# Kernel optimization log

Hardware: AMD Instinct MI355X
Metric: run time of the kernel (lower is better)

The kernel has to match this reference:

```python
import jax, jax.numpy as jnp
import numpy as np
import math

N_EMBD = 1024
N_HEAD = 16
N_CTX = 2048
SCALE = True
NEG = 1e10


def setup_inputs() -> dict:
    key = jax.random.key(0)
    ks = jax.random.split(key, 4)
    B, S = 2, 2048
    x = jax.random.normal(ks[0], (B, S, N_EMBD), dtype=jnp.float32)
    c_attn_w = jax.random.normal(ks[1], (N_EMBD, 3 * N_EMBD), dtype=jnp.float32) * 0.02
    c_attn_b = jnp.zeros((3 * N_EMBD,), dtype=jnp.float32)
    c_proj_w = jax.random.normal(ks[2], (N_EMBD, N_EMBD), dtype=jnp.float32) * 0.02
    c_proj_b = jnp.zeros((N_EMBD,), dtype=jnp.float32)
    return {"x": x, "c_attn_w": c_attn_w, "c_attn_b": c_attn_b,
            "c_proj_w": c_proj_w, "c_proj_b": c_proj_b}


def reference(x, c_attn_w, c_attn_b, c_proj_w, c_proj_b):
    B, S, D = x.shape
    H = N_HEAD
    hd = D // H
    qkv = x @ c_attn_w + c_attn_b                      # [B,S,3D]
    q, k, v = jnp.split(qkv, 3, axis=-1)
    # split heads -> [B,H,S,hd]
    q = q.reshape(B, S, H, hd).transpose(0, 2, 1, 3)
    k = k.reshape(B, S, H, hd).transpose(0, 2, 1, 3)
    v = v.reshape(B, S, H, hd).transpose(0, 2, 1, 3)
    w = jnp.einsum('bhqd,bhkd->bhqk', q, k)           # [B,H,S,S]
    if SCALE:
        w = w / math.sqrt(hd)
    # multiplicative causal mask trick: w*b - 1e10*(1-b)
    b = jnp.tril(jnp.ones((S, S), dtype=w.dtype))[None, None]
    w = w * b - NEG * (1.0 - b)
    w = jax.nn.softmax(w, axis=-1)
    a = jnp.einsum('bhqk,bhkd->bhqd', w, v)           # [B,H,S,hd]
    a = a.transpose(0, 2, 1, 3).reshape(B, S, D)      # merge heads
    a = a @ c_proj_w + c_proj_b
    present = jnp.stack((k, v))                       # [2,B,H,S,hd]
    return a, present
```

## Files before the change

### kernel.cpp

```cpp
#include <hip/hip_runtime.h>
#include <hip/hip_bf16.h>
#include <cstdint>
#include <cstddef>

#define SEQ 2048
#define DMODEL 1024
#define NHEAD 16
#define HDIM 64
#define MTOT 4096
#define NQKV 3072
#define KDIM 1024

#define OUT_K_BASE  4194304u
#define OUT_V_BASE  8388608u

#define QSCALE 0.18033688011112043f

typedef __attribute__((ext_vector_type(4))) float f32x4;
typedef __attribute__((ext_vector_type(8))) __bf16 bf16x8;
typedef __attribute__((ext_vector_type(8))) short s16x8;
typedef __attribute__((ext_vector_type(4))) short s16x4;
typedef __attribute__((ext_vector_type(2))) int i32x2;

static __device__ __forceinline__ unsigned short f2bf(float f) {
  unsigned int u = __builtin_bit_cast(unsigned int, f);
  u += 0x7FFFu + ((u >> 16) & 1u);
  return (unsigned short)(u >> 16);
}

static __device__ __forceinline__ s16x4 pack4(float4 v) {
  s16x4 r;
  r[0] = (short)f2bf(v.x);
  r[1] = (short)f2bf(v.y);
  r[2] = (short)f2bf(v.z);
  r[3] = (short)f2bf(v.w);
  return r;
}

static __device__ __forceinline__ int cvtpk(float lo, float hi) {
  int r;
  asm("v_cvt_pk_bf16_f32 %0, %1, %2" : "=v"(r) : "v"(lo), "v"(hi));
  return r;
}

static __device__ __forceinline__ f32x4 mfma16(s16x8 a, s16x8 b, f32x4 c) {
  return __builtin_amdgcn_mfma_f32_16x16x32_bf16(
      __builtin_bit_cast(bf16x8, a), __builtin_bit_cast(bf16x8, b), c, 0, 0, 0);
}

static __device__ __forceinline__ void gload16(const void* g, void* l) {
  __builtin_amdgcn_global_load_lds(
      (const __attribute__((address_space(1))) unsigned int*)(uintptr_t)g,
      (__attribute__((address_space(3))) unsigned int*)(uintptr_t)l,
      16, 0, 0);
}

#define WAITVM(n) asm volatile("s_waitcnt vmcnt(" #n ")" ::: "memory")

__global__ __launch_bounds__(256) void convert_x(
    const float* __restrict__ X, unsigned short* __restrict__ Xbf)
{
  int i = blockIdx.x * 256 + threadIdx.x;
  float4 v = reinterpret_cast<const float4*>(X)[i];
  reinterpret_cast<s16x4*>(Xbf)[i] = pack4(v);
}

__global__ __launch_bounds__(256) void convert_wt(
    const float* __restrict__ W, unsigned short* __restrict__ Wt, int N)
{
  __shared__ unsigned short t[64][72];
  const int n0 = blockIdx.x * 64, k0 = blockIdx.y * 64;
  const int tid = threadIdx.x;
#pragma unroll
  for (int i = 0; i < 4; ++i) {
    int f = tid + (i << 8);
    int r = f >> 4, c4 = (f & 15) << 2;
    float4 v = *reinterpret_cast<const float4*>(&W[(size_t)(k0 + r) * N + n0 + c4]);
    *reinterpret_cast<s16x4*>(&t[r][c4]) = pack4(v);
  }
  __syncthreads();
#pragma unroll
  for (int i = 0; i < 2; ++i) {
    int g = tid + (i << 8);
    int n = g >> 3, k8 = (g & 7) << 3;
    s16x8 o;
#pragma unroll
    for (int jj = 0; jj < 8; ++jj) o[jj] = (short)t[k8 + jj][n];
    *reinterpret_cast<s16x8*>(&Wt[(size_t)(n0 + n) * KDIM + k0 + k8]) = o;
  }
}

__global__ __launch_bounds__(512, 2) void qkv_gemm(
    const unsigned short* __restrict__ Xbf,
    const unsigned short* __restrict__ Wt,
    const float* __restrict__ Bias,
    float* out,
    unsigned short* __restrict__ Qbf)
{
  __shared__ __align__(16) unsigned short lds_a[2][256][32];
  __shared__ __align__(16) unsigned short lds_b[2][256][32];

  unsigned short* Kbf = (unsigned short*)out;
  unsigned short* Vt  = Kbf + 4194304;

  const int tid = threadIdx.x;
  const int lane = tid & 63;
  const int wv = tid >> 6;
  const int wr = wv >> 2;
  const int wc = wv & 3;
  const int m0 = blockIdx.x * 256;
  const int n0 = blockIdx.y * 256;
  const int lr = lane & 15;
  const int gq = lane >> 4;

  const f32x4 fzero = {0.f, 0.f, 0.f, 0.f};
  f32x4 acc[8][4];
#pragma unroll
  for (int i = 0; i < 8; ++i)
#pragma unroll
    for (int j = 0; j < 4; ++j) acc[i][j] = fzero;

  {
    const int r0 = tid >> 2;
    const int r1 = r0 + 128;
    const int c0 = tid & 3;
    const int sc0 = ((c0 ^ ((r0 >> 1) & 3)) << 3);
    const int sc1 = ((c0 ^ ((r1 >> 1) & 3)) << 3);
    const int ub0 = (wv << 6) << 3;
    const int ub1 = ((1 << 9) + (wv << 6)) << 3;
    auto stage = [&](int nb, int kk) {
      gload16(&Xbf[(size_t)(m0 + r0) * KDIM + kk + sc0], &lds_a[nb][0][0] + ub0);
      gload16(&Xbf[(size_t)(m0 + r1) * KDIM + kk + sc1], &lds_a[nb][0][0] + ub1);
      gload16(&Wt[(size_t)(n0 + r0) * KDIM + kk + sc0], &lds_b[nb][0][0] + ub0);
      gload16(&Wt[(size_t)(n0 + r1) * KDIM + kk + sc1], &lds_b[nb][0][0] + ub1);
    };
    stage(0, 0);
    stage(1, 32);
    for (int t = 0; t < 32; ++t) {
      if (t < 31) { WAITVM(4); } else { WAITVM(0); }
      __builtin_amdgcn_s_barrier();
      const int bufg = t & 1;
      s16x8 bfv[4];
#pragma unroll
      for (int ni = 0; ni < 4; ++ni) {
        int row = wc * 64 + ni * 16 + lr;
        bfv[ni] = *reinterpret_cast<const s16x8*>(
            &lds_b[bufg][row][(gq ^ ((row >> 1) & 3)) << 3]);
      }
      __builtin_amdgcn_s_setprio(1);
#pragma unroll
      for (int mi = 0; mi < 8; ++mi) {
        int row = wr * 128 + mi * 16 + lr;
        s16x8 af = *reinterpret_cast<const s16x8*>(
            &lds_a[bufg][row][(gq ^ ((row >> 1) & 3)) << 3]);
#pragma unroll
        for (int ni = 0; ni < 4; ++ni)
          acc[mi][ni] = mfma16(af, bfv[ni], acc[mi][ni]);
      }
      __builtin_amdgcn_s_setprio(0);
      __builtin_amdgcn_s_barrier();
      if (t < 30) stage(bufg, (t + 2) << 5);
    }
  }

  const int seg = n0 >> 10;

  if (seg == 0) {
#pragma unroll
    for (int ni = 0; ni < 4; ++ni) {
      int c = n0 + wc * 64 + ni * 16 + lr;
      float bias = Bias[c];
      int h = (c & 1023) >> 6, d = c & 63;
#pragma unroll
      for (int mi = 0; mi < 8; ++mi)
#pragma unroll
        for (int j = 0; j < 4; ++j) {
          int m = m0 + wr * 128 + mi * 16 + gq * 4 + j;
          int b = m >> 11, s = m & 2047;
          Qbf[(size_t)((b * NHEAD + h) * SEQ + s) * HDIM + d] =
              f2bf((acc[mi][ni][j] + bias) * QSCALE);
        }
    }
  } else if (seg == 1) {
#pragma unroll
    for (int ni = 0; ni < 4; ++ni) {
      int c = n0 + wc * 64 + ni * 16 + lr;
      float bias = Bias[c];
      int h = (c & 1023) >> 6, d = c & 63;
#pragma unroll
      for (int mi = 0; mi < 8; ++mi)
#pragma unroll
        for (int j = 0; j < 4; ++j) {
          int m = m0 + wr * 128 + mi * 16 + gq * 4 + j;
          int b = m >> 11, s = m & 2047;
          float val = acc[mi][ni][j] + bias;
          size_t idx = (size_t)((b * NHEAD + h) * SEQ + s) * HDIM + d;
          out[OUT_K_BASE + idx] = val;
          Kbf[idx] = f2bf(val);
        }
    }
  } else {
    __syncthreads();
    unsigned short* T = (wv < 4) ? (&lds_a[0][0][0] + (wv << 12))
                                 : (&lds_b[0][0][0] + ((wv - 4) << 12));
    const int b = m0 >> 11;
    const int s0 = (m0 & 2047) + wr * 128;
    const int h = (n0 >> 6) - 32 + wc;
#pragma unroll
    for (int h2 = 0; h2 < 2; ++h2) {
#pragma unroll
      for (int ni = 0; ni < 4; ++ni) {
        int c = n0 + wc * 64 + ni * 16 + lr;
        float bias = Bias[c];
        int d_loc = ni * 16 + lr;
        int dsw = d_loc & 7;
#pragma unroll
        for (int mh = 0; mh < 4; ++mh) {
          int mi = h2 * 4 + mh;
#pragma unroll
          for (int j = 0; j < 4; ++j) {
            int s_loc = mi * 16 + gq * 4 + j;
            int ss = s_loc - (h2 << 6);
            float val = acc[mi][ni][j] + bias;
            out[OUT_V_BASE +
                (size_t)((b * NHEAD + h) * SEQ + s0 + s_loc) * HDIM + d_loc] = val;
            T[d_loc * 64 + (((ss >> 3) ^ dsw) << 3) + (ss & 7)] = f2bf(val);
          }
        }
      }
#pragma unroll
      for (int it = 0; it < 8; ++it) {
        int dl = (lane >> 3) + (it << 3);
        int cl = lane & 7;
        s16x8 vv = *reinterpret_cast<const s16x8*>(
            &T[dl * 64 + ((cl ^ (dl & 7)) << 3)]);
        size_t vi = (((size_t)(b * NHEAD + h) * HDIM + dl) << 11) +
                    s0 + (h2 << 6) + (cl << 3);
        *reinterpret_cast<s16x8*>(&Vt[vi]) = vv;
      }
    }
  }
}

__global__ __launch_bounds__(256) void proj_gemm(
    const unsigned short* __restrict__ Abf,
    const unsigned short* __restrict__ Wpt,
    const float* __restrict__ Bias,
    float* __restrict__ out)
{
  __shared__ __align__(16) unsigned short lds_a[2][128][64];
  __shared__ __align__(16) unsigned short lds_b[2][128][64];

  const int tid = threadIdx.x;
  const int lane = tid & 63;
  const int wv = tid >> 6;
  const int wr = wv >> 1, wc = wv & 1;
  const int m0 = blockIdx.x * 128;
  const int n0 = blockIdx.y * 128;
  const int lr = lane & 15;
  const int gq = lane >> 4;

  const f32x4 fzero = {0.f, 0.f, 0.f, 0.f};
  f32x4 acc[4][4];
#pragma unroll
  for (int i = 0; i < 4; ++i)
#pragma unroll
    for (int j = 0; j < 4; ++j) acc[i][j] = fzero;

  {
    const int r0 = tid >> 3;
    const int c0 = tid & 7;
    auto stage = [&](int nb, int kk) {
#pragma unroll
      for (int i = 0; i < 4; ++i) {
        int r = r0 + (i << 5);
        int sc = ((c0 ^ (r & 7)) << 3);
        int ub = (((i << 8) + (wv << 6)) << 3);
        gload16(&Abf[(size_t)(m0 + r) * KDIM + kk + sc], &lds_a[nb][0][0] + ub);
        gload16(&Wpt[(size_t)(n0 + r) * KDIM + kk + sc], &lds_b[nb][0][0] + ub);
      }
    };
    stage(0, 0);
    stage(1, 64);
    for (int t = 0; t < 16; ++t) {
      if (t < 15) { WAITVM(8); } else { WAITVM(0); }
      __builtin_amdgcn_s_barrier();
      const int bufg = t & 1;
      __builtin_amdgcn_s_setprio(1);
#pragma unroll
      for (int kf = 0; kf < 2; ++kf) {
        s16x8 bfv[4];
#pragma unroll
        for (int ni = 0; ni < 4; ++ni) {
          int row = wc * 64 + ni * 16 + lr;
          bfv[ni] = *reinterpret_cast<const s16x8*>(
              &lds_b[bufg][row][((kf * 4 + gq) ^ (row & 7)) << 3]);
        }
#pragma unroll
        for (int mi = 0; mi < 4; ++mi) {
          int row = wr * 64 + mi * 16 + lr;
          s16x8 af = *reinterpret_cast<const s16x8*>(
              &lds_a[bufg][row][((kf * 4 + gq) ^ (row & 7)) << 3]);
#pragma unroll
          for (int ni = 0; ni < 4; ++ni)
            acc[mi][ni] = mfma16(af, bfv[ni], acc[mi][ni]);
        }
      }
      __builtin_amdgcn_s_setprio(0);
      __builtin_amdgcn_s_barrier();
      if (t < 14) stage(bufg, (t + 2) << 6);
    }
  }

#pragma unroll
  for (int ni = 0; ni < 4; ++ni) {
    int c = n0 + wc * 64 + ni * 16 + lr;
    float bias = Bias[c];
#pragma unroll
    for (int mi = 0; mi < 4; ++mi) {
#pragma unroll
      for (int j = 0; j < 4; ++j) {
        int m = m0 + wr * 64 + mi * 16 + gq * 4 + j;
        out[(size_t)m * DMODEL + c] = acc[mi][ni][j] + bias;
      }
    }
  }
}

__global__ __launch_bounds__(256, 4) void attn_fwd(
    const unsigned short* __restrict__ Qbf,
    const unsigned short* __restrict__ Kbf,
    const unsigned short* __restrict__ Vtg,
    unsigned short* __restrict__ Abf)
{
  __shared__ __align__(16) unsigned short K_lds[2][64][64];
  __shared__ __align__(16) unsigned short V_lds[2][64][64];
  __shared__ __align__(16) unsigned short P_lds[4][16][64];

  const int tid = threadIdx.x;
  const int lane = tid & 63;
  const int wv = tid >> 6;
  const int bid = blockIdx.x;
  const int qt = 31 - (bid >> 5);
  const int bh = bid & 31;

  const int lr = lane & 15;
  const int gq = lane >> 4;

  const unsigned short* Kg = Kbf + (size_t)bh * (SEQ * HDIM);
  const unsigned short* Vg = Vtg + (size_t)bh * (SEQ * HDIM);
  const unsigned short* Qg = Qbf + (size_t)bh * (SEQ * HDIM)
                                 + (size_t)(qt * 64 + wv * 16) * HDIM;

  s16x8 qf0 = *reinterpret_cast<const s16x8*>(&Qg[lr * 64 + (gq << 3)]);
  s16x8 qf1 = *reinterpret_cast<const s16x8*>(&Qg[lr * 64 + 32 + (gq << 3)]);

  const f32x4 fzero = {0.f, 0.f, 0.f, 0.f};
  f32x4 O[4];
  float mrow = -1e30f, lrow = 0.f;
#pragma unroll
  for (int no = 0; no < 4; ++no) O[no] = fzero;

#define STAGE(kv0, nb)                                                        \
  {                                                                           \
    _Pragma("unroll")                                                         \
    for (int i = 0; i < 2; ++i) {                                             \
      int L = tid + (i << 8);                                                 \
      int r = L >> 3, c = L & 7;                                              \
      int cc = (c ^ (r & 7)) << 3;                                            \
      int ubase = ((i << 8) + (wv << 6)) << 3;                                \
      gload16(&Kg[(((kv0) + r) << 6) + cc], &K_lds[nb][0][0] + ubase);        \
      gload16(&Vg[((size_t)r << 11) + (kv0) + cc], &V_lds[nb][0][0] + ubase); \
    }                                                                         \
  }

  STAGE(0, 0);

  for (int t = 0; t <= qt; ++t) {
    __syncthreads();
    if (t < qt) STAGE((t + 1) * 64, (t + 1) & 1);
    const int buf = t & 1;

    f32x4 sc[4];
#pragma unroll
    for (int ni = 0; ni < 4; ++ni) {
      int kr = ni * 16 + lr;
      int sw = kr & 7;
      s16x8 kb0 = *reinterpret_cast<const s16x8*>(&K_lds[buf][kr][(gq ^ sw) << 3]);
      s16x8 kb1 = *reinterpret_cast<const s16x8*>(&K_lds[buf][kr][((gq + 4) ^ sw) << 3]);
      f32x4 tacc = mfma16(kb0, qf0, fzero);
      sc[ni] = mfma16(kb1, qf1, tacc);
    }

    if (t == qt) {
      int qloc = wv * 16 + lr;
#pragma unroll
      for (int ni = 0; ni < 4; ++ni)
#pragma unroll
        for (int r = 0; r < 4; ++r)
          if (ni * 16 + gq * 4 + r > qloc) sc[ni][r] = -1e30f;
    }

    float tmax = fmaxf(fmaxf(fmaxf(sc[0][0], sc[0][1]), fmaxf(sc[0][2], sc[0][3])),
                       fmaxf(fmaxf(sc[1][0], sc[1][1]), fmaxf(sc[1][2], sc[1][3])));
    tmax = fmaxf(tmax,
                 fmaxf(fmaxf(fmaxf(sc[2][0], sc[2][1]), fmaxf(sc[2][2], sc[2][3])),
                       fmaxf(fmaxf(sc[3][0], sc[3][1]), fmaxf(sc[3][2], sc[3][3]))));
    tmax = fmaxf(tmax, __shfl_xor(tmax, 16));
    tmax = fmaxf(tmax, __shfl_xor(tmax, 32));
    float newm = fmaxf(mrow, tmax);
    float fs = __builtin_amdgcn_exp2f(mrow - newm);
    mrow = newm;
    float rs = 0.f;
#pragma unroll
    for (int ni = 0; ni < 4; ++ni) {
#pragma unroll
      for (int r = 0; r < 4; ++r) {
        float p = __builtin_amdgcn_exp2f(sc[ni][r] - newm);
        sc[ni][r] = p;
        rs += p;
      }
    }
    rs += __shfl_xor(rs, 16);
    rs += __shfl_xor(rs, 32);
    lrow = lrow * fs + rs;
#pragma unroll
    for (int no = 0; no < 4; ++no) O[no] *= fs;

    {
      unsigned short* Prow = &P_lds[wv][lr][0];
      const int swl = lr & 7;
#pragma unroll
      for (int ni = 0; ni < 4; ++ni) {
        i32x2 d2;
        d2[0] = cvtpk(sc[ni][0], sc[ni][1]);
        d2[1] = cvtpk(sc[ni][2], sc[ni][3]);
        int off = ((((2 * ni) + (gq >> 1)) ^ swl) << 3) + ((gq & 1) << 2);
        *reinterpret_cast<i32x2*>(&Prow[off]) = d2;
      }
      s16x8 pB0 = *reinterpret_cast<const s16x8*>(&Prow[(gq ^ swl) << 3]);
      s16x8 pB1 = *reinterpret_cast<const s16x8*>(&Prow[((gq + 4) ^ swl) << 3]);

#pragma unroll
      for (int no = 0; no < 4; ++no) {
        int dr = no * 16 + lr;
        int sw = dr & 7;
        s16x8 vb0 = *reinterpret_cast<const s16x8*>(&V_lds[buf][dr][(gq ^ sw) << 3]);
        s16x8 vb1 = *reinterpret_cast<const s16x8*>(&V_lds[buf][dr][((gq + 4) ^ sw) << 3]);
        O[no] = mfma16(vb0, pB0, O[no]);
        O[no] = mfma16(vb1, pB1, O[no]);
      }
    }
  }

  const int b = bh >> 4, h = bh & 15;
  float inv = 1.0f / lrow;
  int srow = qt * 64 + wv * 16 + lr;
  size_t base = (size_t)(b * SEQ + srow) * DMODEL + h * 64 + (gq << 2);
#pragma unroll
  for (int no = 0; no < 4; ++no) {
    s16x4 ov;
#pragma unroll
    for (int r = 0; r < 4; ++r) ov[r] = (short)f2bf(O[no][r] * inv);
    *reinterpret_cast<s16x4*>(&Abf[base + no * 16]) = ov;
  }
#undef STAGE
}

extern "C" void kernel_launch(void* const* d_in, const int* in_sizes, int n_in,
                              void* d_out, int out_size, void* d_ws, size_t ws_size,
                              hipStream_t stream) {
  const float* x        = (const float*)d_in[0];
  const float* c_attn_w = (const float*)d_in[1];
  const float* c_attn_b = (const float*)d_in[2];
  const float* c_proj_w = (const float*)d_in[3];
  const float* c_proj_b = (const float*)d_in[4];
  float* out = (float*)d_out;

  unsigned short* Qbf = (unsigned short*)d_ws;
  unsigned short* Xbf = Qbf + 4194304;
  unsigned short* Abf = Xbf;
  unsigned short* Wt  = Qbf + 8388608;
  unsigned short* Wpt = Wt;
  unsigned short* Kbf = (unsigned short*)out;
  unsigned short* Vt  = Kbf + 4194304;

  convert_x<<<dim3(4096), 256, 0, stream>>>(x, Xbf);
  convert_wt<<<dim3(48, 16), 256, 0, stream>>>(c_attn_w, Wt, NQKV);
  qkv_gemm<<<dim3(16, 12), 512, 0, stream>>>(Xbf, Wt, c_attn_b, out, Qbf);
  convert_wt<<<dim3(16, 16), 256, 0, stream>>>(c_proj_w, Wpt, DMODEL);
  attn_fwd<<<dim3(1024), 256, 0, stream>>>(Qbf, Kbf, Vt, Abf);
  proj_gemm<<<dim3(32, 8), 256, 0, stream>>>(Abf, Wpt, c_proj_b, out);
}
```

Before: 113.4 us.

## Triple-buffer QKV GEMM LDS and interleave staged loads with MFMA phases

Moves the QKV GEMM main loop from double to triple buffering in LDS. Each k-step is split into two half-phases that read LDS fragments, issue part of the next-next tile's global-to-LDS loads, and then run the MFMAs between barriers. The aim is to hide global load latency and spread load issue across compute. In exchange, LDS use rises from 64KB to 96KB per block, which may block two blocks per CU, and each k-step now carries more barriers. The epilogue's LDS transpose scratch pointers are remapped to the new array sizes.

```diff
diff --git a/kernel.cpp b/kernel.cpp
--- a/kernel.cpp
+++ b/kernel.cpp
@@ -56,6 +56,7 @@
 }
 
 #define WAITVM(n) asm volatile("s_waitcnt vmcnt(" #n ")" ::: "memory")
+#define SBAR() asm volatile("s_barrier" ::: "memory")
 
 __global__ __launch_bounds__(256) void convert_x(
     const float* __restrict__ X, unsigned short* __restrict__ Xbf)
@@ -97,8 +98,8 @@
     float* out,
     unsigned short* __restrict__ Qbf)
 {
-  __shared__ __align__(16) unsigned short lds_a[2][256][32];
-  __shared__ __align__(16) unsigned short lds_b[2][256][32];
+  __shared__ __align__(16) unsigned short lds_a[3][256][32];
+  __shared__ __align__(16) unsigned short lds_b[3][256][32];
 
   unsigned short* Kbf = (unsigned short*)out;
   unsigned short* Vt  = Kbf + 4194304;
@@ -121,45 +122,68 @@
     for (int j = 0; j < 4; ++j) acc[i][j] = fzero;
 
   {
-    const int r0 = tid >> 2;
-    const int r1 = r0 + 128;
-    const int c0 = tid & 3;
-    const int sc0 = ((c0 ^ ((r0 >> 1) & 3)) << 3);
-    const int sc1 = ((c0 ^ ((r1 >> 1) & 3)) << 3);
-    const int ub0 = (wv << 6) << 3;
-    const int ub1 = ((1 << 9) + (wv << 6)) << 3;
-    auto stage = [&](int nb, int kk) {
-      gload16(&Xbf[(size_t)(m0 + r0) * KDIM + kk + sc0], &lds_a[nb][0][0] + ub0);
-      gload16(&Xbf[(size_t)(m0 + r1) * KDIM + kk + sc1], &lds_a[nb][0][0] + ub1);
-      gload16(&Wt[(size_t)(n0 + r0) * KDIM + kk + sc0], &lds_b[nb][0][0] + ub0);
-      gload16(&Wt[(size_t)(n0 + r1) * KDIM + kk + sc1], &lds_b[nb][0][0] + ub1);
+    const int sr  = tid >> 2;
+    const int ssc = ((tid & 3) ^ ((sr >> 1) & 3)) << 3;
+    const int ub  = (wv << 6) << 3;
+
+    auto stageA = [&](int nb, int kt) {
+      int kk = kt << 5;
+      gload16(&Xbf[(size_t)(m0 + sr) * KDIM + kk + ssc],
+              &lds_a[nb][0][0] + ub);
+      gload16(&Xbf[(size_t)(m0 + 128 + sr) * KDIM + kk + ssc],
+              &lds_a[nb][128][0] + ub);
     };
-    stage(0, 0);
-    stage(1, 32);
-    for (int t = 0; t < 32; ++t) {
-      if (t < 31) { WAITVM(4); } else { WAITVM(0); }
-      __builtin_amdgcn_s_barrier();
-      const int bufg = t & 1;
-      s16x8 bfv[4];
-#pragma unroll
-      for (int ni = 0; ni < 4; ++ni) {
-        int row = wc * 64 + ni * 16 + lr;
-        bfv[ni] = *reinterpret_cast<const s16x8*>(
-            &lds_b[bufg][row][(gq ^ ((row >> 1) & 3)) << 3]);
-      }
-      __builtin_amdgcn_s_setprio(1);
-#pragma unroll
-      for (int mi = 0; mi < 8; ++mi) {
-        int row = wr * 128 + mi * 16 + lr;
-        s16x8 af = *reinterpret_cast<const s16x8*>(
-            &lds_a[bufg][row][(gq ^ ((row >> 1) & 3)) << 3]);
-#pragma unroll
-        for (int ni = 0; ni < 4; ++ni)
-          acc[mi][ni] = mfma16(af, bfv[ni], acc[mi][ni]);
-      }
-      __builtin_amdgcn_s_setprio(0);
-      __builtin_amdgcn_s_barrier();
-      if (t < 30) stage(bufg, (t + 2) << 5);
+    auto stageB = [&](int nb, int kt) {
+      int kk = kt << 5;
+      gload16(&Wt[(size_t)(n0 + sr) * KDIM + kk + ssc],
+              &lds_b[nb][0][0] + ub);
+      gload16(&Wt[(size_t)(n0 + 128 + sr) * KDIM + kk + ssc],
+              &lds_b[nb][128][0] + ub);
+    };
+
+    stageA(0, 0); stageB(0, 0);
+    stageA(1, 1); stageB(1, 1);
+    WAITVM(4);
+    SBAR();
+
+    int buf = 0;
+    int sbuf = 2;
+    for (int kt = 0; kt < 32; ++kt) {
+#pragma unroll
+      for (int q = 0; q < 2; ++q) {
+        s16x8 af[4], bfv[4];
+#pragma unroll
+        for (int ml = 0; ml < 4; ++ml) {
+          int row = wr * 128 + (q * 4 + ml) * 16 + lr;
+          af[ml] = *reinterpret_cast<const s16x8*>(
+              &lds_a[buf][row][(gq ^ ((row >> 1) & 3)) << 3]);
+        }
+#pragma unroll
+        for (int ni = 0; ni < 4; ++ni) {
+          int row = wc * 64 + ni * 16 + lr;
+          bfv[ni] = *reinterpret_cast<const s16x8*>(
+              &lds_b[buf][row][(gq ^ ((row >> 1) & 3)) << 3]);
+        }
+        if (kt < 30) {
+          if (q == 0) stageA(sbuf, kt + 2);
+          else        stageB(sbuf, kt + 2);
+        }
+        if (q == 1) {
+          if (kt < 30)       { WAITVM(4); }
+          else if (kt == 30) { WAITVM(0); }
+        }
+        SBAR();
+        __builtin_amdgcn_s_setprio(1);
+#pragma unroll
+        for (int ml = 0; ml < 4; ++ml)
+#pragma unroll
+          for (int ni = 0; ni < 4; ++ni)
+            acc[q * 4 + ml][ni] = mfma16(af[ml], bfv[ni], acc[q * 4 + ml][ni]);
+        __builtin_amdgcn_s_setprio(0);
+        SBAR();
+      }
+      buf = (buf == 2) ? 0 : buf + 1;
+      sbuf = (sbuf == 2) ? 0 : sbuf + 1;
     }
   }
 
@@ -201,8 +225,8 @@
     }
   } else {
     __syncthreads();
-    unsigned short* T = (wv < 4) ? (&lds_a[0][0][0] + (wv << 12))
-                                 : (&lds_b[0][0][0] + ((wv - 4) << 12));
+    unsigned short* T = (wv < 6) ? (&lds_a[0][0][0] + (wv << 12))
+                                 : (&lds_b[0][0][0] + ((wv - 6) << 12));
     const int b = m0 >> 11;
     const int s0 = (m0 & 2047) + wr * 128;
     const int h = (n0 >> 6) - 32 + wc;
```

Result: no change. 114.9 us (+1.3%).

## Retile QKV GEMM to 128x128 blocks and move fp32 K/V output into a separate kernel

Applied to the files above, without the earlier changes.

The QKV GEMM moves from 256x256 tiles with 512 threads to 128x128 tiles with 256 threads and a K-step of 64. That gives 768 blocks instead of 192, so the grid fills the CUs better. The Q and K epilogues now go through an LDS transpose, producing coalesced 16-byte bf16 stores in place of scattered 2-byte ones. The fp32 `present` K/V writes leave the GEMM and go to a new expand_kv kernel, which rebuilds them from the bf16 copies. This costs an extra launch and extra memory traffic, and the fp32 K/V output is now bf16-rounded, which could affect accuracy.

```diff
diff --git a/kernel.cpp b/kernel.cpp
--- a/kernel.cpp
+++ b/kernel.cpp
@@ -28,6 +28,11 @@
   return (unsigned short)(u >> 16);
 }
 
+static __device__ __forceinline__ float bf2f(unsigned short u) {
+  unsigned int x = ((unsigned int)u) << 16;
+  return __builtin_bit_cast(float, x);
+}
+
 static __device__ __forceinline__ s16x4 pack4(float4 v) {
   s16x4 r;
   r[0] = (short)f2bf(v.x);
@@ -90,155 +95,188 @@
   }
 }
 
-__global__ __launch_bounds__(512, 2) void qkv_gemm(
+__global__ __launch_bounds__(256) void qkv_gemm(
     const unsigned short* __restrict__ Xbf,
     const unsigned short* __restrict__ Wt,
     const float* __restrict__ Bias,
-    float* out,
-    unsigned short* __restrict__ Qbf)
+    unsigned short* __restrict__ Qbf,
+    unsigned short* __restrict__ Kbf,
+    unsigned short* __restrict__ Vt)
 {
-  __shared__ __align__(16) unsigned short lds_a[2][256][32];
-  __shared__ __align__(16) unsigned short lds_b[2][256][32];
-
-  unsigned short* Kbf = (unsigned short*)out;
-  unsigned short* Vt  = Kbf + 4194304;
+  __shared__ __align__(16) unsigned short lds_a[2][128][64];
+  __shared__ __align__(16) unsigned short lds_b[2][128][64];
 
   const int tid = threadIdx.x;
   const int lane = tid & 63;
   const int wv = tid >> 6;
-  const int wr = wv >> 2;
-  const int wc = wv & 3;
-  const int m0 = blockIdx.x * 256;
-  const int n0 = blockIdx.y * 256;
+  const int wr = wv >> 1, wc = wv & 1;
+  const int m0 = blockIdx.x * 128;
+  const int n0 = blockIdx.y * 128;
   const int lr = lane & 15;
   const int gq = lane >> 4;
 
   const f32x4 fzero = {0.f, 0.f, 0.f, 0.f};
-  f32x4 acc[8][4];
-#pragma unroll
-  for (int i = 0; i < 8; ++i)
+  f32x4 acc[4][4];
+#pragma unroll
+  for (int i = 0; i < 4; ++i)
 #pragma unroll
     for (int j = 0; j < 4; ++j) acc[i][j] = fzero;
 
   {
-    const int r0 = tid >> 2;
-    const int r1 = r0 + 128;
-    const int c0 = tid & 3;
-    const int sc0 = ((c0 ^ ((r0 >> 1) & 3)) << 3);
-    const int sc1 = ((c0 ^ ((r1 >> 1) & 3)) << 3);
-    const int ub0 = (wv << 6) << 3;
-    const int ub1 = ((1 << 9) + (wv << 6)) << 3;
+    const int r0 = tid >> 3;
+    const int c0 = tid & 7;
     auto stage = [&](int nb, int kk) {
-      gload16(&Xbf[(size_t)(m0 + r0) * KDIM + kk + sc0], &lds_a[nb][0][0] + ub0);
-      gload16(&Xbf[(size_t)(m0 + r1) * KDIM + kk + sc1], &lds_a[nb][0][0] + ub1);
-      gload16(&Wt[(size_t)(n0 + r0) * KDIM + kk + sc0], &lds_b[nb][0][0] + ub0);
-      gload16(&Wt[(size_t)(n0 + r1) * KDIM + kk + sc1], &lds_b[nb][0][0] + ub1);
+#pragma unroll
+      for (int i = 0; i < 4; ++i) {
+        int r = r0 + (i << 5);
+        int sc = ((c0 ^ (r & 7)) << 3);
+        int ub = (((i << 8) + (wv << 6)) << 3);
+        gload16(&Xbf[(size_t)(m0 + r) * KDIM + kk + sc], &lds_a[nb][0][0] + ub);
+        gload16(&Wt[(size_t)(n0 + r) * KDIM + kk + sc], &lds_b[nb][0][0] + ub);
+      }
     };
     stage(0, 0);
-    stage(1, 32);
-    for (int t = 0; t < 32; ++t) {
-      if (t < 31) { WAITVM(4); } else { WAITVM(0); }
+    stage(1, 64);
+    for (int t = 0; t < 16; ++t) {
+      if (t < 15) { WAITVM(8); } else { WAITVM(0); }
       __builtin_amdgcn_s_barrier();
       const int bufg = t & 1;
-      s16x8 bfv[4];
-#pragma unroll
-      for (int ni = 0; ni < 4; ++ni) {
-        int row = wc * 64 + ni * 16 + lr;
-        bfv[ni] = *reinterpret_cast<const s16x8*>(
-            &lds_b[bufg][row][(gq ^ ((row >> 1) & 3)) << 3]);
-      }
       __builtin_amdgcn_s_setprio(1);
 #pragma unroll
-      for (int mi = 0; mi < 8; ++mi) {
-        int row = wr * 128 + mi * 16 + lr;
-        s16x8 af = *reinterpret_cast<const s16x8*>(
-            &lds_a[bufg][row][(gq ^ ((row >> 1) & 3)) << 3]);
-#pragma unroll
-        for (int ni = 0; ni < 4; ++ni)
-          acc[mi][ni] = mfma16(af, bfv[ni], acc[mi][ni]);
+      for (int kf = 0; kf < 2; ++kf) {
+        s16x8 bfv[4];
+#pragma unroll
+        for (int ni = 0; ni < 4; ++ni) {
+          int row = wc * 64 + ni * 16 + lr;
+          bfv[ni] = *reinterpret_cast<const s16x8*>(
+              &lds_b[bufg][row][((kf * 4 + gq) ^ (row & 7)) << 3]);
+        }
+#pragma unroll
+        for (int mi = 0; mi < 4; ++mi) {
+          int row = wr * 64 + mi * 16 + lr;
+          s16x8 af = *reinterpret_cast<const s16x8*>(
+              &lds_a[bufg][row][((kf * 4 + gq) ^ (row & 7)) << 3]);
+#pragma unroll
+          for (int ni = 0; ni < 4; ++ni)
+            acc[mi][ni] = mfma16(af, bfv[ni], acc[mi][ni]);
+        }
       }
       __builtin_amdgcn_s_setprio(0);
       __builtin_amdgcn_s_barrier();
-      if (t < 30) stage(bufg, (t + 2) << 5);
-    }
-  }
-
+      if (t < 14) stage(bufg, (t + 2) << 6);
+    }
+  }
+
+  __syncthreads();
+  unsigned short* T = (wv < 2) ? (&lds_a[0][0][0] + (wv << 12))
+                               : (&lds_b[0][0][0] + ((wv - 2) << 12));
   const int seg = n0 >> 10;
-
-  if (seg == 0) {
+  const int b = m0 >> 11;
+  const int s0 = (m0 & 2047) + wr * 64;
+  const int h = ((n0 & 1023) >> 6) + wc;
+  const size_t bh = (size_t)(b * NHEAD + h);
+
+  if (seg <= 1) {
 #pragma unroll
     for (int ni = 0; ni < 4; ++ni) {
       int c = n0 + wc * 64 + ni * 16 + lr;
       float bias = Bias[c];
-      int h = (c & 1023) >> 6, d = c & 63;
-#pragma unroll
-      for (int mi = 0; mi < 8; ++mi)
+      int ch = 2 * ni + (lr >> 3);
+      int el = lr & 7;
+#pragma unroll
+      for (int mi = 0; mi < 4; ++mi)
 #pragma unroll
         for (int j = 0; j < 4; ++j) {
-          int m = m0 + wr * 128 + mi * 16 + gq * 4 + j;
-          int b = m >> 11, s = m & 2047;
-          Qbf[(size_t)((b * NHEAD + h) * SEQ + s) * HDIM + d] =
-              f2bf((acc[mi][ni][j] + bias) * QSCALE);
+          int s_loc = mi * 16 + gq * 4 + j;
+          float val = acc[mi][ni][j] + bias;
+          if (seg == 0) val *= QSCALE;
+          T[s_loc * 64 + ((ch ^ (s_loc & 7)) << 3) + el] = f2bf(val);
         }
     }
-  } else if (seg == 1) {
+    unsigned short* dst = (seg == 0) ? Qbf : Kbf;
+#pragma unroll
+    for (int it = 0; it < 8; ++it) {
+      int rr = (lane >> 3) + (it << 3);
+      int cl = lane & 7;
+      s16x8 vv = *reinterpret_cast<const s16x8*>(
+          &T[rr * 64 + ((cl ^ (rr & 7)) << 3)]);
+      *reinterpret_cast<s16x8*>(
+          &dst[(bh * SEQ + s0 + rr) * HDIM + (cl << 3)]) = vv;
+    }
+  } else {
 #pragma unroll
     for (int ni = 0; ni < 4; ++ni) {
       int c = n0 + wc * 64 + ni * 16 + lr;
       float bias = Bias[c];
-      int h = (c & 1023) >> 6, d = c & 63;
-#pragma unroll
-      for (int mi = 0; mi < 8; ++mi)
+      int d_loc = ni * 16 + lr;
+      int dsw = d_loc & 7;
+#pragma unroll
+      for (int mi = 0; mi < 4; ++mi)
 #pragma unroll
         for (int j = 0; j < 4; ++j) {
-          int m = m0 + wr * 128 + mi * 16 + gq * 4 + j;
-          int b = m >> 11, s = m & 2047;
-          float val = acc[mi][ni][j] + bias;
-          size_t idx = (size_t)((b * NHEAD + h) * SEQ + s) * HDIM + d;
-          out[OUT_K_BASE + idx] = val;
-          Kbf[idx] = f2bf(val);
+          int s_loc = mi * 16 + gq * 4 + j;
+          T[d_loc * 64 + (((s_loc >> 3) ^ dsw) << 3) + (s_loc & 7)] =
+              f2bf(acc[mi][ni][j] + bias);
         }
     }
-  } else {
-    __syncthreads();
-    unsigned short* T = (wv < 4) ? (&lds_a[0][0][0] + (wv << 12))
-                                 : (&lds_b[0][0][0] + ((wv - 4) << 12));
-    const int b = m0 >> 11;
-    const int s0 = (m0 & 2047) + wr * 128;
-    const int h = (n0 >> 6) - 32 + wc;
-#pragma unroll
-    for (int h2 = 0; h2 < 2; ++h2) {
-#pragma unroll
-      for (int ni = 0; ni < 4; ++ni) {
-        int c = n0 + wc * 64 + ni * 16 + lr;
-        float bias = Bias[c];
-        int d_loc = ni * 16 + lr;
-        int dsw = d_loc & 7;
-#pragma unroll
-        for (int mh = 0; mh < 4; ++mh) {
-          int mi = h2 * 4 + mh;
-#pragma unroll
-          for (int j = 0; j < 4; ++j) {
-            int s_loc = mi * 16 + gq * 4 + j;
-            int ss = s_loc - (h2 << 6);
-            float val = acc[mi][ni][j] + bias;
-            out[OUT_V_BASE +
-                (size_t)((b * NHEAD + h) * SEQ + s0 + s_loc) * HDIM + d_loc] = val;
-            T[d_loc * 64 + (((ss >> 3) ^ dsw) << 3) + (ss & 7)] = f2bf(val);
-          }
-        }
-      }
-#pragma unroll
-      for (int it = 0; it < 8; ++it) {
-        int dl = (lane >> 3) + (it << 3);
-        int cl = lane & 7;
-        s16x8 vv = *reinterpret_cast<const s16x8*>(
-            &T[dl * 64 + ((cl ^ (dl & 7)) << 3)]);
-        size_t vi = (((size_t)(b * NHEAD + h) * HDIM + dl) << 11) +
-                    s0 + (h2 << 6) + (cl << 3);
-        *reinterpret_cast<s16x8*>(&Vt[vi]) = vv;
-      }
-    }
+#pragma unroll
+    for (int it = 0; it < 8; ++it) {
+      int dl = (lane >> 3) + (it << 3);
+      int cl = lane & 7;
+      s16x8 vv = *reinterpret_cast<const s16x8*>(
+          &T[dl * 64 + ((cl ^ (dl & 7)) << 3)]);
+      *reinterpret_cast<s16x8*>(
+          &Vt[(bh * HDIM + dl) * SEQ + s0 + (cl << 3)]) = vv;
+    }
+  }
+}
+
+__global__ __launch_bounds__(256) void expand_kv(
+    const unsigned short* __restrict__ Kbf,
+    const unsigned short* __restrict__ Vtg,
+    float* __restrict__ out)
+{
+  __shared__ unsigned short T[64][72];
+  const int tid = threadIdx.x;
+  const int s0 = blockIdx.x * 64;
+  const int bh = blockIdx.y;
+
+#pragma unroll
+  for (int i = 0; i < 2; ++i) {
+    int idx = tid + (i << 8);
+    int r = idx >> 3, dc = (idx & 7) << 3;
+    size_t off = ((size_t)bh * SEQ + s0 + r) * HDIM + dc;
+    s16x8 kv = *reinterpret_cast<const s16x8*>(&Kbf[off]);
+    float4 lo = {bf2f((unsigned short)kv[0]), bf2f((unsigned short)kv[1]),
+                 bf2f((unsigned short)kv[2]), bf2f((unsigned short)kv[3])};
+    float4 hi = {bf2f((unsigned short)kv[4]), bf2f((unsigned short)kv[5]),
+                 bf2f((unsigned short)kv[6]), bf2f((unsigned short)kv[7])};
+    *reinterpret_cast<float4*>(&out[OUT_K_BASE + off]) = lo;
+    *reinterpret_cast<float4*>(&out[OUT_K_BASE + off + 4]) = hi;
+  }
+
+#pragma unroll
+  for (int i = 0; i < 2; ++i) {
+    int idx = tid + (i << 8);
+    int d = idx >> 3, sc = idx & 7;
+    s16x8 vv = *reinterpret_cast<const s16x8*>(
+        &Vtg[((size_t)bh * HDIM + d) * SEQ + s0 + (sc << 3)]);
+#pragma unroll
+    for (int e = 0; e < 8; ++e) T[sc * 8 + e][d] = (unsigned short)vv[e];
+  }
+  __syncthreads();
+#pragma unroll
+  for (int i = 0; i < 2; ++i) {
+    int idx = tid + (i << 8);
+    int sr = idx >> 3, dc = (idx & 7) << 3;
+    s16x8 vv = *reinterpret_cast<const s16x8*>(&T[sr][dc]);
+    float4 lo = {bf2f((unsigned short)vv[0]), bf2f((unsigned short)vv[1]),
+                 bf2f((unsigned short)vv[2]), bf2f((unsigned short)vv[3])};
+    float4 hi = {bf2f((unsigned short)vv[4]), bf2f((unsigned short)vv[5]),
+                 bf2f((unsigned short)vv[6]), bf2f((unsigned short)vv[7])};
+    size_t off = ((size_t)bh * SEQ + s0 + sr) * HDIM + dc;
+    *reinterpret_cast<float4*>(&out[OUT_V_BASE + off]) = lo;
+    *reinterpret_cast<float4*>(&out[OUT_V_BASE + off + 4]) = hi;
   }
 }
 
@@ -487,7 +525,8 @@
 
   convert_x<<<dim3(4096), 256, 0, stream>>>(x, Xbf);
   convert_wt<<<dim3(48, 16), 256, 0, stream>>>(c_attn_w, Wt, NQKV);
-  qkv_gemm<<<dim3(16, 12), 512, 0, stream>>>(Xbf, Wt, c_attn_b, out, Qbf);
+  qkv_gemm<<<dim3(32, 24), 256, 0, stream>>>(Xbf, Wt, c_attn_b, Qbf, Kbf, Vt);
+  expand_kv<<<dim3(32, 32), 256, 0, stream>>>(Kbf, Vt, out);
   convert_wt<<<dim3(16, 16), 256, 0, stream>>>(c_proj_w, Wpt, DMODEL);
   attn_fwd<<<dim3(1024), 256, 0, stream>>>(Qbf, Kbf, Vt, Abf);
   proj_gemm<<<dim3(32, 8), 256, 0, stream>>>(Abf, Wpt, c_proj_b, out);
```

Measured after the change: 116.1 us. +2.3%, slower.
